# Kernel optimization log

Hardware: AMD Instinct MI355X
Metric: run time of the kernel (lower is better)

The kernel has to match this reference:

```python
import jax, jax.numpy as jnp
import numpy as np

EPS = 1e-5  # torch InstanceNorm2d / LayerNorm default eps


def setup_inputs() -> dict:
    key = jax.random.key(0)
    k1, k2, k3 = jax.random.split(key, 3)
    B, C, H, W_ = 8, 256, 128, 128
    x = jax.random.normal(k1, (B, C, H, W_), dtype=jnp.float32)
    params = jax.random.normal(k2, (B, 2 * C), dtype=jnp.float32)
    # Conv2d(dim*2, dim, 1) weight, squeezed to [C_out, C_in]
    W = jax.random.normal(k3, (C, 2 * C), dtype=jnp.float32) * (1.0 / np.sqrt(2 * C))
    return {"x": x, "params": params, "W": W}


def reference(x, params, W):
    # x: [B, C, H, W]; params: [B, 2C]; W: [C, 2C]
    C = x.shape[1]
    # InstanceNorm2d (no affine): normalize over spatial dims per (b, c), biased var
    in_mean = jnp.mean(x, axis=(2, 3), keepdims=True)
    in_var = jnp.var(x, axis=(2, 3), keepdims=True)
    IN = (x - in_mean) * jax.lax.rsqrt(in_var + EPS)
    # LayerNorm over (C, H, W) per sample, biased var
    ln_mean = jnp.mean(x, axis=(1, 2, 3), keepdims=True)
    ln_var = jnp.var(x, axis=(1, 2, 3), keepdims=True)
    LN = (x - ln_mean) * jax.lax.rsqrt(ln_var + EPS)
    LIN = jnp.concatenate((IN, LN), axis=1)  # [B, 2C, H, W]
    # 1x1 conv == channel contraction
    c = jnp.einsum('bihw,oi->bohw', LIN, W)  # [B, C, H, W]
    gamma = params[:, :C][:, :, None, None]
    beta = params[:, C:][:, :, None, None]
    return gamma * c + beta
```

## Files before the change

kernel.cpp:

```cpp
#include <hip/hip_runtime.h>
#include <stdint.h>

#define HW_  16384
#define CH   256
#define NB   8
#define EPSV 1e-5f

typedef float f32x4 __attribute__((ext_vector_type(4)));
typedef short s16x8 __attribute__((ext_vector_type(8)));

__device__ __forceinline__ unsigned short f2bf(float f) {
    union { float f; uint32_t u; } v; v.f = f;
    uint32_t r = (v.u + 0x7FFFu + ((v.u >> 16) & 1u)) >> 16;
    return (unsigned short)r;
}

__device__ __forceinline__ void glds16(const unsigned short* g, unsigned short* l) {
    __builtin_amdgcn_global_load_lds(
        (const __attribute__((address_space(1))) uint32_t*)g,
        (__attribute__((address_space(3))) uint32_t*)l,
        16, 0, 0);
}

__global__ __launch_bounds__(256) void stats_kernel(const float* __restrict__ x,
                                                    float* __restrict__ sums,
                                                    float* __restrict__ sumsq) {
    const int bc  = blockIdx.x;
    const int tid = threadIdx.x;
    const float4* p = reinterpret_cast<const float4*>(x + (size_t)bc * HW_);
    float s = 0.f, q = 0.f;
#pragma unroll 4
    for (int i = tid; i < HW_ / 4; i += 256) {
        float4 v = p[i];
        s += v.x + v.y + v.z + v.w;
        q += v.x * v.x + v.y * v.y + v.z * v.z + v.w * v.w;
    }
    __shared__ float rs[256], rq[256];
    rs[tid] = s; rq[tid] = q;
    __syncthreads();
    for (int off = 128; off > 0; off >>= 1) {
        if (tid < off) { rs[tid] += rs[tid + off]; rq[tid] += rq[tid + off]; }
        __syncthreads();
    }
    if (tid == 0) { sums[bc] = rs[0]; sumsq[bc] = rq[0]; }
}

__global__ __launch_bounds__(256) void prep_kernel(const float* __restrict__ sums,
                                                   const float* __restrict__ sumsq,
                                                   const float* __restrict__ params,
                                                   const float* __restrict__ W,
                                                   unsigned short* __restrict__ Atile,
                                                   float* __restrict__ Dp) {
    const int b   = blockIdx.x;
    const int tid = threadIdx.x;
    __shared__ float mu[CH], ri[CH], rs[CH], rq[CH];
    float s = sums[b * CH + tid];
    float q = sumsq[b * CH + tid];
    float m = s * (1.0f / HW_);
    float v = q * (1.0f / HW_) - m * m;
    mu[tid] = m;
    ri[tid] = rsqrtf(v + EPSV);
    rs[tid] = s; rq[tid] = q;
    __syncthreads();
    for (int off = 128; off > 0; off >>= 1) {
        if (tid < off) { rs[tid] += rs[tid + off]; rq[tid] += rq[tid + off]; }
        __syncthreads();
    }
    const float invN = 1.0f / ((float)CH * (float)HW_);
    const float mln  = rs[0] * invN;
    const float vln  = rq[0] * invN - mln * mln;
    const float rln  = rsqrtf(vln + EPSV);

    const int o = tid;
    const float gamma = params[b * 2 * CH + o];
    const float beta  = params[b * 2 * CH + CH + o];
    const float4* w1p = reinterpret_cast<const float4*>(W + (size_t)o * 2 * CH);
    const float4* w2p = reinterpret_cast<const float4*>(W + (size_t)o * 2 * CH + CH);
    unsigned short* ab = Atile + (size_t)b * (8 * 4 * 256 * 8);
    float t1 = 0.f, t2 = 0.f;
    for (int c4 = 0; c4 < CH / 4; ++c4) {
        float4 w1 = w1p[c4];
        float4 w2 = w2p[c4];
        float w1a[4] = {w1.x, w1.y, w1.z, w1.w};
        float w2a[4] = {w2.x, w2.y, w2.z, w2.w};
        const int c = c4 * 4;
        ushort4 pk;
        unsigned short* pka = (unsigned short*)&pk;
#pragma unroll
        for (int j = 0; j < 4; ++j) {
            float ric = ri[c + j];
            float a   = gamma * (w1a[j] * ric + w2a[j] * rln);
            pka[j] = f2bf(a);
            t1 += w1a[j] * ric * mu[c + j];
            t2 += w2a[j];
        }
        const int kb = c >> 5, g = (c >> 3) & 3, e0 = c & 4;
        *reinterpret_cast<ushort4*>(&ab[(size_t)(((kb * 4 + g) * 256 + o) * 8 + e0)]) = pk;
    }
    const float d = -(t1 + rln * mln * t2);
    Dp[b * CH + o] = gamma * d + beta;
}

__global__ __launch_bounds__(512, 4) void gemm_kernel(const float* __restrict__ x,
                                                      const unsigned short* __restrict__ Atile,
                                                      const float* __restrict__ Dp,
                                                      float* __restrict__ out) {
    __shared__ unsigned short As[2][4 * 256 * 8];
    __shared__ unsigned short Xs[2][4 * 128 * 8];

    const int b   = blockIdx.y;
    const int n0  = blockIdx.x * 128;
    const int t   = threadIdx.x;
    const int w   = t >> 6;
    const int l   = t & 63;
    const int wm  = w >> 1;
    const int wn  = w & 1;
    const int lhi = l >> 4;
    const int llo = l & 15;

    f32x4 acc[4][4];
    const float* dpb = Dp + b * CH;
#pragma unroll
    for (int fm = 0; fm < 4; ++fm) {
        f32x4 d = *reinterpret_cast<const f32x4*>(dpb + wm * 64 + fm * 16 + lhi * 4);
#pragma unroll
        for (int fn = 0; fn < 4; ++fn) acc[fm][fn] = d;
    }

    const size_t xbase = (size_t)b * CH * HW_ + n0;
    const unsigned short* apb = Atile + (size_t)b * (8 * 4 * 256 * 8);
    uint32_t* Xs32 = reinterpret_cast<uint32_t*>(&Xs[0][0]);

    const int i0 = 2 * w,      i1 = 2 * w + 1;
    const int g0 = i0 & 3,     q0 = i0 >> 2;
    const int g1 = i1 & 3,     q1 = i1 >> 2;
    const unsigned short* aglob0 = apb + (size_t)(g0 * 256 + q0 * 64 + l) * 8;
    const unsigned short* aglob1 = apb + (size_t)(g1 * 256 + q1 * 64 + l) * 8;
    unsigned short* alds0 = &As[0][g0 * 2048 + q0 * 512];
    unsigned short* alds1 = &As[0][g1 * 2048 + q1 * 512];

    const int kp = t >> 5;
    const int nq = t & 31;
    const int xg = kp >> 2;
    const int xh = kp & 3;
    const float* xlane = x + xbase + (size_t)(2 * kp) * HW_ + nq * 4;

    int npr[4];
#pragma unroll
    for (int fn = 0; fn < 4; ++fn) {
        const int nr = wn * 64 + fn * 16 + llo;
        npr[fn] = nr ^ ((nr >> 3) & 7);
    }

    glds16(aglob0, alds0);
    glds16(aglob1, alds1);
    f32x4 xa[2], xb[2];
    xa[0] = *reinterpret_cast<const f32x4*>(xlane);
    xb[0] = *reinterpret_cast<const f32x4*>(xlane + HW_);
    xa[1] = *reinterpret_cast<const f32x4*>(xlane + (size_t)32 * HW_);
    xb[1] = *reinterpret_cast<const f32x4*>(xlane + (size_t)32 * HW_ + HW_);
#pragma unroll
    for (int j = 0; j < 4; ++j) {
        const int n  = nq * 4 + j;
        const int np = n ^ ((n >> 3) & 7);
        Xs32[xg * 512 + np * 4 + xh] =
            (uint32_t)f2bf(xa[0][j]) | ((uint32_t)f2bf(xb[0][j]) << 16);
    }

#pragma unroll
    for (int kb = 0; kb < 8; ++kb) {
        const int cur = kb & 1, nxt = cur ^ 1;

        if (kb == 7) {
            asm volatile("s_waitcnt vmcnt(0) lgkmcnt(0)" ::: "memory");
        } else {
            asm volatile("s_waitcnt vmcnt(2) lgkmcnt(0)" ::: "memory");
        }
        __builtin_amdgcn_s_barrier();

        if (kb < 7) {
            glds16(aglob0 + (kb + 1) * 8192, alds0 + nxt * 8192);
            glds16(aglob1 + (kb + 1) * 8192, alds1 + nxt * 8192);
        }
        if (kb < 6) {
            const float* xp = xlane + (size_t)(kb + 2) * 32 * HW_;
            xa[cur] = *reinterpret_cast<const f32x4*>(xp);
            xb[cur] = *reinterpret_cast<const f32x4*>(xp + HW_);
        }

        s16x8 af[4];
#pragma unroll
        for (int fm = 0; fm < 4; ++fm)
            af[fm] = *reinterpret_cast<const s16x8*>(&As[cur][lhi * 2048 + (wm * 64 + fm * 16 + llo) * 8]);
#pragma unroll
        for (int fn = 0; fn < 4; ++fn) {
            s16x8 bfr = *reinterpret_cast<const s16x8*>(&Xs[cur][lhi * 1024 + npr[fn] * 8]);
#pragma unroll
            for (int fm = 0; fm < 4; ++fm)
                acc[fm][fn] = __builtin_amdgcn_mfma_f32_16x16x32_bf16(af[fm], bfr, acc[fm][fn], 0, 0, 0);
        }

        if (kb < 7) {
#pragma unroll
            for (int j = 0; j < 4; ++j) {
                const int n  = nq * 4 + j;
                const int np = n ^ ((n >> 3) & 7);
                Xs32[nxt * 2048 + xg * 512 + np * 4 + xh] =
                    (uint32_t)f2bf(xa[nxt][j]) | ((uint32_t)f2bf(xb[nxt][j]) << 16);
            }
        }
    }

#pragma unroll
    for (int fm = 0; fm < 4; ++fm) {
        const int m = wm * 64 + fm * 16 + lhi * 4;
        float* obase = out + (size_t)(b * CH + m) * HW_ + n0 + wn * 64 + llo;
#pragma unroll
        for (int fn = 0; fn < 4; ++fn) {
#pragma unroll
            for (int r = 0; r < 4; ++r)
                obase[(size_t)r * HW_ + fn * 16] = acc[fm][fn][r];
        }
    }
}

extern "C" void kernel_launch(void* const* d_in, const int* in_sizes, int n_in,
                              void* d_out, int out_size, void* d_ws, size_t ws_size,
                              hipStream_t stream) {
    const float* x      = (const float*)d_in[0];
    const float* params = (const float*)d_in[1];
    const float* W      = (const float*)d_in[2];
    float* out = (float*)d_out;
    float* ws  = (float*)d_ws;

    float* sums  = ws;
    float* sumsq = ws + 2048;
    float* Dp    = ws + 4096;
    unsigned short* Atile = (unsigned short*)(ws + 6144);

    hipLaunchKernelGGL(stats_kernel, dim3(NB * CH), dim3(256), 0, stream, x, sums, sumsq);
    hipLaunchKernelGGL(prep_kernel,  dim3(NB),      dim3(256), 0, stream, sums, sumsq, params, W, Atile, Dp);
    hipLaunchKernelGGL(gemm_kernel,  dim3(HW_ / 128, NB), dim3(512), 0, stream, x, Atile, Dp, out);
}
```

Before: 96.75 us.

## Fuse bf16 packing of x into stats pass and feed GEMM packed input

The statistics kernel now also converts x to bf16 and writes channel-pair-interleaved 32-bit words to a workspace buffer. The GEMM then reads this half-size packed tensor instead of fp32 x and no longer converts in its inner loop. This cuts GEMM read traffic and conversion ALU work, but adds a 64MB write and a 64MB read of the packed buffer. The net memory traffic goes up, so the benefit depends on whether the GEMM was latency- or conversion-bound.

```diff
diff --git a/kernel.cpp b/kernel.cpp
--- a/kernel.cpp
+++ b/kernel.cpp
@@ -1,4 +1,5 @@
 #include <hip/hip_runtime.h>
+#include <hip/hip_bf16.h>
 #include <stdint.h>
 
 #define HW_  16384
@@ -8,11 +9,18 @@
 
 typedef float f32x4 __attribute__((ext_vector_type(4)));
 typedef short s16x8 __attribute__((ext_vector_type(8)));
+typedef uint32_t u32x4 __attribute__((ext_vector_type(4)));
 
 __device__ __forceinline__ unsigned short f2bf(float f) {
     union { float f; uint32_t u; } v; v.f = f;
     uint32_t r = (v.u + 0x7FFFu + ((v.u >> 16) & 1u)) >> 16;
     return (unsigned short)r;
+}
+
+__device__ __forceinline__ uint32_t pkbf(float lo, float hi) {
+    __hip_bfloat162 h = __float22bfloat162_rn(make_float2(lo, hi));
+    union { __hip_bfloat162 h; uint32_t u; } v; v.h = h;
+    return v.u;
 }
 
 __device__ __forceinline__ void glds16(const unsigned short* g, unsigned short* l) {
@@ -22,27 +30,47 @@
         16, 0, 0);
 }
 
-__global__ __launch_bounds__(256) void stats_kernel(const float* __restrict__ x,
-                                                    float* __restrict__ sums,
-                                                    float* __restrict__ sumsq) {
-    const int bc  = blockIdx.x;
+__global__ __launch_bounds__(256) void pack_kernel(const float* __restrict__ x,
+                                                   uint32_t* __restrict__ xp,
+                                                   float* __restrict__ sums,
+                                                   float* __restrict__ sumsq) {
+    const int bcp = blockIdx.x;
     const int tid = threadIdx.x;
-    const float4* p = reinterpret_cast<const float4*>(x + (size_t)bc * HW_);
-    float s = 0.f, q = 0.f;
+    const f32x4* pa = reinterpret_cast<const f32x4*>(x + (size_t)(2 * bcp) * HW_);
+    const f32x4* pb = reinterpret_cast<const f32x4*>(x + (size_t)(2 * bcp + 1) * HW_);
+    u32x4* dst = reinterpret_cast<u32x4*>(xp + (size_t)bcp * HW_);
+
+    float sA = 0.f, qA = 0.f, sB = 0.f, qB = 0.f;
 #pragma unroll 4
     for (int i = tid; i < HW_ / 4; i += 256) {
-        float4 v = p[i];
-        s += v.x + v.y + v.z + v.w;
-        q += v.x * v.x + v.y * v.y + v.z * v.z + v.w * v.w;
-    }
-    __shared__ float rs[256], rq[256];
-    rs[tid] = s; rq[tid] = q;
+        f32x4 va = pa[i], vb = pb[i];
+        sA += va[0] + va[1] + va[2] + va[3];
+        qA += va[0]*va[0] + va[1]*va[1] + va[2]*va[2] + va[3]*va[3];
+        sB += vb[0] + vb[1] + vb[2] + vb[3];
+        qB += vb[0]*vb[0] + vb[1]*vb[1] + vb[2]*vb[2] + vb[3]*vb[3];
+        u32x4 o;
+        o[0] = pkbf(va[0], vb[0]);
+        o[1] = pkbf(va[1], vb[1]);
+        o[2] = pkbf(va[2], vb[2]);
+        o[3] = pkbf(va[3], vb[3]);
+        dst[i] = o;
+    }
+    __shared__ float r0[256], r1[256], r2[256], r3[256];
+    r0[tid] = sA; r1[tid] = qA; r2[tid] = sB; r3[tid] = qB;
     __syncthreads();
     for (int off = 128; off > 0; off >>= 1) {
-        if (tid < off) { rs[tid] += rs[tid + off]; rq[tid] += rq[tid + off]; }
+        if (tid < off) {
+            r0[tid] += r0[tid + off]; r1[tid] += r1[tid + off];
+            r2[tid] += r2[tid + off]; r3[tid] += r3[tid + off];
+        }
         __syncthreads();
     }
-    if (tid == 0) { sums[bc] = rs[0]; sumsq[bc] = rq[0]; }
+    if (tid == 0) {
+        sums [2 * bcp    ] = r0[0];
+        sumsq[2 * bcp    ] = r1[0];
+        sums [2 * bcp + 1] = r2[0];
+        sumsq[2 * bcp + 1] = r3[0];
+    }
 }
 
 __global__ __launch_bounds__(256) void prep_kernel(const float* __restrict__ sums,
@@ -101,7 +129,7 @@
     Dp[b * CH + o] = gamma * d + beta;
 }
 
-__global__ __launch_bounds__(512, 4) void gemm_kernel(const float* __restrict__ x,
+__global__ __launch_bounds__(512, 4) void gemm_kernel(const uint32_t* __restrict__ xp,
                                                       const unsigned short* __restrict__ Atile,
                                                       const float* __restrict__ Dp,
                                                       float* __restrict__ out) {
@@ -127,7 +155,6 @@
         for (int fn = 0; fn < 4; ++fn) acc[fm][fn] = d;
     }
 
-    const size_t xbase = (size_t)b * CH * HW_ + n0;
     const unsigned short* apb = Atile + (size_t)b * (8 * 4 * 256 * 8);
     uint32_t* Xs32 = reinterpret_cast<uint32_t*>(&Xs[0][0]);
 
@@ -143,7 +170,7 @@
     const int nq = t & 31;
     const int xg = kp >> 2;
     const int xh = kp & 3;
-    const float* xlane = x + xbase + (size_t)(2 * kp) * HW_ + nq * 4;
+    const uint32_t* xlane = xp + (size_t)(b * 128 + kp) * HW_ + n0 + nq * 4;
 
     int npr[4];
 #pragma unroll
@@ -154,17 +181,14 @@
 
     glds16(aglob0, alds0);
     glds16(aglob1, alds1);
-    f32x4 xa[2], xb[2];
-    xa[0] = *reinterpret_cast<const f32x4*>(xlane);
-    xb[0] = *reinterpret_cast<const f32x4*>(xlane + HW_);
-    xa[1] = *reinterpret_cast<const f32x4*>(xlane + (size_t)32 * HW_);
-    xb[1] = *reinterpret_cast<const f32x4*>(xlane + (size_t)32 * HW_ + HW_);
+    u32x4 xv[2];
+    xv[0] = *reinterpret_cast<const u32x4*>(xlane);
+    xv[1] = *reinterpret_cast<const u32x4*>(xlane + (size_t)16 * HW_);
 #pragma unroll
     for (int j = 0; j < 4; ++j) {
         const int n  = nq * 4 + j;
         const int np = n ^ ((n >> 3) & 7);
-        Xs32[xg * 512 + np * 4 + xh] =
-            (uint32_t)f2bf(xa[0][j]) | ((uint32_t)f2bf(xb[0][j]) << 16);
+        Xs32[xg * 512 + np * 4 + xh] = xv[0][j];
     }
 
 #pragma unroll
@@ -174,7 +198,7 @@
         if (kb == 7) {
             asm volatile("s_waitcnt vmcnt(0) lgkmcnt(0)" ::: "memory");
         } else {
-            asm volatile("s_waitcnt vmcnt(2) lgkmcnt(0)" ::: "memory");
+            asm volatile("s_waitcnt vmcnt(1) lgkmcnt(0)" ::: "memory");
         }
         __builtin_amdgcn_s_barrier();
 
@@ -183,9 +207,7 @@
             glds16(aglob1 + (kb + 1) * 8192, alds1 + nxt * 8192);
         }
         if (kb < 6) {
-            const float* xp = xlane + (size_t)(kb + 2) * 32 * HW_;
-            xa[cur] = *reinterpret_cast<const f32x4*>(xp);
-            xb[cur] = *reinterpret_cast<const f32x4*>(xp + HW_);
+            xv[cur] = *reinterpret_cast<const u32x4*>(xlane + (size_t)(kb + 2) * 16 * HW_);
         }
 
         s16x8 af[4];
@@ -205,8 +227,7 @@
             for (int j = 0; j < 4; ++j) {
                 const int n  = nq * 4 + j;
                 const int np = n ^ ((n >> 3) & 7);
-                Xs32[nxt * 2048 + xg * 512 + np * 4 + xh] =
-                    (uint32_t)f2bf(xa[nxt][j]) | ((uint32_t)f2bf(xb[nxt][j]) << 16);
+                Xs32[nxt * 2048 + xg * 512 + np * 4 + xh] = xv[nxt][j];
             }
         }
     }
@@ -231,14 +252,15 @@
     const float* params = (const float*)d_in[1];
     const float* W      = (const float*)d_in[2];
     float* out = (float*)d_out;
-    float* ws  = (float*)d_ws;
-
-    float* sums  = ws;
-    float* sumsq = ws + 2048;
-    float* Dp    = ws + 4096;
-    unsigned short* Atile = (unsigned short*)(ws + 6144);
-
-    hipLaunchKernelGGL(stats_kernel, dim3(NB * CH), dim3(256), 0, stream, x, sums, sumsq);
-    hipLaunchKernelGGL(prep_kernel,  dim3(NB),      dim3(256), 0, stream, sums, sumsq, params, W, Atile, Dp);
-    hipLaunchKernelGGL(gemm_kernel,  dim3(HW_ / 128, NB), dim3(512), 0, stream, x, Atile, Dp, out);
-}
+    char*  ws  = (char*)d_ws;
+
+    float*          sums  = (float*)(ws);
+    float*          sumsq = (float*)(ws + (1u << 20));
+    float*          Dp    = (float*)(ws + (2u << 20));
+    unsigned short* Atile = (unsigned short*)(ws + (3u << 20));
+    uint32_t*       xp    = (uint32_t*)(ws + (8u << 20));
+
+    hipLaunchKernelGGL(pack_kernel, dim3(NB * 128), dim3(256), 0, stream, x, xp, sums, sumsq);
+    hipLaunchKernelGGL(prep_kernel, dim3(NB),       dim3(256), 0, stream, sums, sumsq, params, W, Atile, Dp);
+    hipLaunchKernelGGL(gemm_kernel, dim3(HW_ / 128, NB), dim3(512), 0, stream, xp, Atile, Dp, out);
+}
```

After: 110.1 us. +13.8%, slower.

## Halve GEMM N-tile to 64 columns and raise occupancy target

Applied to the files above, without the earlier changes.

The GEMM tile along the spatial dimension shrinks from 128 to 64 columns, so there are twice as many workgroups, each with half the accumulators and half the X staging in shared memory. The launch-bounds occupancy hint rises from 4 to 6 blocks, and the hand-tuned s_waitcnt plus barrier becomes a plain __syncthreads. The aim is more resident waves and more blocks to hide memory latency. In exchange the A tile (all 256 output rows) is re-read from global twice as often, X loads shrink to 8-byte vectors, and the new barrier waits for all outstanding loads each iteration, which weakens the prefetch overlap.

```diff
diff --git a/kernel.cpp b/kernel.cpp
--- a/kernel.cpp
+++ b/kernel.cpp
@@ -7,6 +7,7 @@
 #define EPSV 1e-5f
 
 typedef float f32x4 __attribute__((ext_vector_type(4)));
+typedef float f32x2 __attribute__((ext_vector_type(2)));
 typedef short s16x8 __attribute__((ext_vector_type(8)));
 
 __device__ __forceinline__ unsigned short f2bf(float f) {
@@ -101,15 +102,15 @@
     Dp[b * CH + o] = gamma * d + beta;
 }
 
-__global__ __launch_bounds__(512, 4) void gemm_kernel(const float* __restrict__ x,
+__global__ __launch_bounds__(512, 6) void gemm_kernel(const float* __restrict__ x,
                                                       const unsigned short* __restrict__ Atile,
                                                       const float* __restrict__ Dp,
                                                       float* __restrict__ out) {
     __shared__ unsigned short As[2][4 * 256 * 8];
-    __shared__ unsigned short Xs[2][4 * 128 * 8];
+    __shared__ unsigned short Xs[2][4 * 64 * 8];
 
     const int b   = blockIdx.y;
-    const int n0  = blockIdx.x * 128;
+    const int n0  = blockIdx.x * 64;
     const int t   = threadIdx.x;
     const int w   = t >> 6;
     const int l   = t & 63;
@@ -118,16 +119,14 @@
     const int lhi = l >> 4;
     const int llo = l & 15;
 
-    f32x4 acc[4][4];
+    f32x4 acc[4][2];
     const float* dpb = Dp + b * CH;
 #pragma unroll
     for (int fm = 0; fm < 4; ++fm) {
         f32x4 d = *reinterpret_cast<const f32x4*>(dpb + wm * 64 + fm * 16 + lhi * 4);
-#pragma unroll
-        for (int fn = 0; fn < 4; ++fn) acc[fm][fn] = d;
-    }
-
-    const size_t xbase = (size_t)b * CH * HW_ + n0;
+        acc[fm][0] = d; acc[fm][1] = d;
+    }
+
     const unsigned short* apb = Atile + (size_t)b * (8 * 4 * 256 * 8);
     uint32_t* Xs32 = reinterpret_cast<uint32_t*>(&Xs[0][0]);
 
@@ -140,43 +139,37 @@
     unsigned short* alds1 = &As[0][g1 * 2048 + q1 * 512];
 
     const int kp = t >> 5;
-    const int nq = t & 31;
+    const int n2 = (t & 31) * 2;
     const int xg = kp >> 2;
     const int xh = kp & 3;
-    const float* xlane = x + xbase + (size_t)(2 * kp) * HW_ + nq * 4;
-
-    int npr[4];
-#pragma unroll
-    for (int fn = 0; fn < 4; ++fn) {
-        const int nr = wn * 64 + fn * 16 + llo;
+    const float* xlane = x + (size_t)b * CH * HW_ + (size_t)(2 * kp) * HW_ + n0 + n2;
+
+    int npr[2];
+#pragma unroll
+    for (int fn = 0; fn < 2; ++fn) {
+        const int nr = wn * 32 + fn * 16 + llo;
         npr[fn] = nr ^ ((nr >> 3) & 7);
     }
 
     glds16(aglob0, alds0);
     glds16(aglob1, alds1);
-    f32x4 xa[2], xb[2];
-    xa[0] = *reinterpret_cast<const f32x4*>(xlane);
-    xb[0] = *reinterpret_cast<const f32x4*>(xlane + HW_);
-    xa[1] = *reinterpret_cast<const f32x4*>(xlane + (size_t)32 * HW_);
-    xb[1] = *reinterpret_cast<const f32x4*>(xlane + (size_t)32 * HW_ + HW_);
-#pragma unroll
-    for (int j = 0; j < 4; ++j) {
-        const int n  = nq * 4 + j;
+    f32x2 xa[2], xb[2];
+    xa[0] = *reinterpret_cast<const f32x2*>(xlane);
+    xb[0] = *reinterpret_cast<const f32x2*>(xlane + HW_);
+    xa[1] = *reinterpret_cast<const f32x2*>(xlane + (size_t)32 * HW_);
+    xb[1] = *reinterpret_cast<const f32x2*>(xlane + (size_t)32 * HW_ + HW_);
+#pragma unroll
+    for (int j = 0; j < 2; ++j) {
+        const int n  = n2 + j;
         const int np = n ^ ((n >> 3) & 7);
-        Xs32[xg * 512 + np * 4 + xh] =
+        Xs32[xg * 256 + np * 4 + xh] =
             (uint32_t)f2bf(xa[0][j]) | ((uint32_t)f2bf(xb[0][j]) << 16);
     }
 
 #pragma unroll
     for (int kb = 0; kb < 8; ++kb) {
+        __syncthreads();
         const int cur = kb & 1, nxt = cur ^ 1;
-
-        if (kb == 7) {
-            asm volatile("s_waitcnt vmcnt(0) lgkmcnt(0)" ::: "memory");
-        } else {
-            asm volatile("s_waitcnt vmcnt(2) lgkmcnt(0)" ::: "memory");
-        }
-        __builtin_amdgcn_s_barrier();
 
         if (kb < 7) {
             glds16(aglob0 + (kb + 1) * 8192, alds0 + nxt * 8192);
@@ -184,8 +177,8 @@
         }
         if (kb < 6) {
             const float* xp = xlane + (size_t)(kb + 2) * 32 * HW_;
-            xa[cur] = *reinterpret_cast<const f32x4*>(xp);
-            xb[cur] = *reinterpret_cast<const f32x4*>(xp + HW_);
+            xa[cur] = *reinterpret_cast<const f32x2*>(xp);
+            xb[cur] = *reinterpret_cast<const f32x2*>(xp + HW_);
         }
 
         s16x8 af[4];
@@ -193,8 +186,8 @@
         for (int fm = 0; fm < 4; ++fm)
             af[fm] = *reinterpret_cast<const s16x8*>(&As[cur][lhi * 2048 + (wm * 64 + fm * 16 + llo) * 8]);
 #pragma unroll
-        for (int fn = 0; fn < 4; ++fn) {
-            s16x8 bfr = *reinterpret_cast<const s16x8*>(&Xs[cur][lhi * 1024 + npr[fn] * 8]);
+        for (int fn = 0; fn < 2; ++fn) {
+            s16x8 bfr = *reinterpret_cast<const s16x8*>(&Xs[cur][lhi * 512 + npr[fn] * 8]);
 #pragma unroll
             for (int fm = 0; fm < 4; ++fm)
                 acc[fm][fn] = __builtin_amdgcn_mfma_f32_16x16x32_bf16(af[fm], bfr, acc[fm][fn], 0, 0, 0);
@@ -202,10 +195,10 @@
 
         if (kb < 7) {
 #pragma unroll
-            for (int j = 0; j < 4; ++j) {
-                const int n  = nq * 4 + j;
+            for (int j = 0; j < 2; ++j) {
+                const int n  = n2 + j;
                 const int np = n ^ ((n >> 3) & 7);
-                Xs32[nxt * 2048 + xg * 512 + np * 4 + xh] =
+                Xs32[nxt * 1024 + xg * 256 + np * 4 + xh] =
                     (uint32_t)f2bf(xa[nxt][j]) | ((uint32_t)f2bf(xb[nxt][j]) << 16);
             }
         }
@@ -214,9 +207,9 @@
 #pragma unroll
     for (int fm = 0; fm < 4; ++fm) {
         const int m = wm * 64 + fm * 16 + lhi * 4;
-        float* obase = out + (size_t)(b * CH + m) * HW_ + n0 + wn * 64 + llo;
-#pragma unroll
-        for (int fn = 0; fn < 4; ++fn) {
+        float* obase = out + (size_t)(b * CH + m) * HW_ + n0 + wn * 32 + llo;
+#pragma unroll
+        for (int fn = 0; fn < 2; ++fn) {
 #pragma unroll
             for (int r = 0; r < 4; ++r)
                 obase[(size_t)r * HW_ + fn * 16] = acc[fm][fn][r];
@@ -240,5 +233,5 @@
 
     hipLaunchKernelGGL(stats_kernel, dim3(NB * CH), dim3(256), 0, stream, x, sums, sumsq);
     hipLaunchKernelGGL(prep_kernel,  dim3(NB),      dim3(256), 0, stream, sums, sumsq, params, W, Atile, Dp);
-    hipLaunchKernelGGL(gemm_kernel,  dim3(HW_ / 128, NB), dim3(512), 0, stream, x, Atile, Dp, out);
-}
+    hipLaunchKernelGGL(gemm_kernel,  dim3(HW_ / 64, NB), dim3(512), 0, stream, x, Atile, Dp, out);
+}
```

Result: slower. 100.3 us (+3.7%).
